# Optimization experiments

Measured on AMD Instinct MI355X. Metric: run time of the kernel, lower is better.

## Reference

```python
import jax, jax.numpy as jnp
import numpy as np

N, E, IN, ED, H, L, OUT = 50000, 600000, 16, 4, 128, 4, 3


def setup_inputs() -> dict:
    key = jax.random.key(0)
    ks = jax.random.split(key, 16)
    s = 0.05  # small init scale for numerical stability
    return {
        "x": jax.random.normal(ks[0], (N, IN), jnp.float32),
        "edge_index": jax.random.randint(ks[1], (2, E), 0, N, jnp.int64 if jax.config.jax_enable_x64 else jnp.int32),
        "edge_attr": jax.random.normal(ks[2], (E, ED), jnp.float32),
        "lin_in_w": jax.random.normal(ks[3], (IN, H), jnp.float32) * s,
        "lin_in_b": jnp.zeros((H,), jnp.float32),
        "msg_w1": jax.random.normal(ks[4], (L, H + ED, H), jnp.float32) * s,
        "msg_b1": jnp.zeros((L, H), jnp.float32),
        "msg_w2": jax.random.normal(ks[5], (L, H, H), jnp.float32) * s,
        "msg_b2": jnp.zeros((L, H), jnp.float32),
        "upd_w1": jax.random.normal(ks[6], (L, 2 * H, H), jnp.float32) * s,
        "upd_b1": jnp.zeros((L, H), jnp.float32),
        "upd_w2": jax.random.normal(ks[7], (L, H, H), jnp.float32) * s,
        "upd_b2": jnp.zeros((L, H), jnp.float32),
        "head_w1": jax.random.normal(ks[8], (H, H), jnp.float32) * s,
        "head_b1": jnp.zeros((H,), jnp.float32),
        "head_w2": jax.random.normal(ks[9], (H, OUT), jnp.float32) * s,
        "head_b2": jnp.zeros((OUT,), jnp.float32),
    }


def reference(x, edge_index, edge_attr, lin_in_w, lin_in_b,
              msg_w1, msg_b1, msg_w2, msg_b2,
              upd_w1, upd_b1, upd_w2, upd_b2,
              head_w1, head_b1, head_w2, head_b2):
    n = x.shape[0]
    src, dst = edge_index[0], edge_index[1]  # PyG: message from src (x_j), aggregate at dst
    h = jax.nn.relu(x @ lin_in_w + lin_in_b)  # [N, H]
    # mean-aggregation denominator (0-degree nodes -> divide by 1, sum is 0 anyway)
    cnt = jax.ops.segment_sum(jnp.ones((src.shape[0],), h.dtype), dst, num_segments=n)
    cnt = jnp.maximum(cnt, 1.0)[:, None]
    for l in range(msg_w1.shape[0]):
        mi = jnp.concatenate([h[src], edge_attr], axis=1)          # [E, H+ED] edge gather
        m = jax.nn.relu(mi @ msg_w1[l] + msg_b1[l])
        m = jax.nn.relu(m @ msg_w2[l] + msg_b2[l])                 # [E, H] per-edge message
        agg = jax.ops.segment_sum(m, dst, num_segments=n) / cnt    # [N, H] scatter-mean
        u = jnp.concatenate([h, agg], axis=1)
        u = jax.nn.relu(u @ upd_w1[l] + upd_b1[l])
        u = u @ upd_w2[l] + upd_b2[l]
        h = jax.nn.relu(u + h)  # residual + relu; dropout is eval-mode identity
    o = jax.nn.relu(h @ head_w1 + head_b1)
    return jax.nn.relu(o @ head_w2 + head_b2)  # [N, OUT]
```

## Files before the change

### kernel.cpp

```cpp
#include <hip/hip_runtime.h>


typedef _Float16 f16x8 __attribute__((ext_vector_type(8)));
typedef _Float16 f16x2 __attribute__((ext_vector_type(2)));
typedef __fp16  fp16x2 __attribute__((ext_vector_type(2)));
typedef float f32x4 __attribute__((ext_vector_type(4)));

__device__ inline uint pk2(float a, float b) {
  fp16x2 h = __builtin_amdgcn_cvt_pkrtz(a, b);
  return __builtin_bit_cast(uint, h);
}
__device__ inline ushort f2h(float f) {
  fp16x2 h = __builtin_amdgcn_cvt_pkrtz(f, 0.f);
  return (ushort)__builtin_bit_cast(uint, h);
}
__device__ inline f16x2 bch(uint u) { return __builtin_bit_cast(f16x2, u); }

template <int NT>
__device__ inline void stage_w(ushort* Ws, const ushort* __restrict__ Wt, int t) {
#pragma unroll
  for (int i = t; i < 2048; i += NT) {
    int r = i >> 4, c = i & 15;
    *(uint4*)&Ws[r * 136 + c * 8] = *(const uint4*)&Wt[r * 128 + c * 8];
  }
}
__device__ inline void mfma_4ks(f32x4* acc, const ushort* A, const ushort* Ws,
                                int wave, int lane) {
  int cl = lane & 15, kq = (lane >> 4) * 8;
  int arow = (wave * 16 + cl) * 136;
#pragma unroll
  for (int ks = 0; ks < 4; ++ks) {
    f16x8 af = *(const f16x8*)&A[arow + ks * 32 + kq];
#pragma unroll
    for (int ct = 0; ct < 8; ++ct) {
      f16x8 bf = *(const f16x8*)&Ws[(ct * 16 + cl) * 136 + ks * 32 + kq];
      acc[ct] = __builtin_amdgcn_mfma_f32_16x16x32_f16(af, bf, acc[ct], 0, 0, 0);
    }
  }
}
__device__ inline void mfma_regA(f32x4* acc, const f16x8* af, const ushort* Ws,
                                 int lane) {
  int cl = lane & 15, kq = (lane >> 4) * 8;
#pragma unroll
  for (int ks = 0; ks < 4; ++ks) {
#pragma unroll
    for (int ct = 0; ct < 8; ++ct) {
      f16x8 bf = *(const f16x8*)&Ws[(ct * 16 + cl) * 136 + ks * 32 + kq];
      acc[ct] = __builtin_amdgcn_mfma_f32_16x16x32_f16(af[ks], bf, acc[ct], 0, 0, 0);
    }
  }
}

__global__ __launch_bounds__(256) void count_int_kernel(const int* __restrict__ dst,
                                                        int* __restrict__ cnti, int E) {
  int e = blockIdx.x * 256 + threadIdx.x;
  if (e < E) atomicAdd(&cnti[dst[e]], 1);
}

__global__ __launch_bounds__(256) void scan_block_sum(const int* __restrict__ cnti,
                                                      int* __restrict__ bsum, int N) {
  int i = blockIdx.x * 256 + threadIdx.x;
  int v = (i < N) ? cnti[i] : 0;
#pragma unroll
  for (int o = 1; o < 64; o <<= 1) v += __shfl_xor(v, o);
  __shared__ int wsum[4];
  if ((threadIdx.x & 63) == 0) wsum[threadIdx.x >> 6] = v;
  __syncthreads();
  if (threadIdx.x == 0) bsum[blockIdx.x] = wsum[0] + wsum[1] + wsum[2] + wsum[3];
}
__global__ __launch_bounds__(256) void scan_partials(int* __restrict__ bsum, int nb) {
  __shared__ int s[256];
  int t = threadIdx.x;
  int v = (t < nb) ? bsum[t] : 0;
  s[t] = v;
  __syncthreads();
  for (int o = 1; o < 256; o <<= 1) {
    int u = (t >= o) ? s[t - o] : 0;
    __syncthreads();
    s[t] += u;
    __syncthreads();
  }
  if (t < nb) bsum[t] = s[t] - v;
}
__global__ __launch_bounds__(256) void scan_final(const int* __restrict__ cnti,
                                                  const int* __restrict__ bsum,
                                                  int* __restrict__ rowptr,
                                                  float* __restrict__ invf, int N) {
  __shared__ int s[256];
  int i = blockIdx.x * 256 + threadIdx.x;
  int t = threadIdx.x;
  int v = (i < N) ? cnti[i] : 0;
  s[t] = v;
  __syncthreads();
  for (int o = 1; o < 256; o <<= 1) {
    int u = (t >= o) ? s[t - o] : 0;
    __syncthreads();
    s[t] += u;
    __syncthreads();
  }
  if (i < N) {
    rowptr[i] = bsum[blockIdx.x] + s[t] - v;
    invf[i] = 1.f / (float)max(v, 1);
  }
}

__global__ __launch_bounds__(256) void scatter_kernel(
    const int* __restrict__ src, const int* __restrict__ dst,
    const float4* __restrict__ ea, const int* __restrict__ rowptr,
    int* __restrict__ tmpc, int* __restrict__ srcs, int* __restrict__ dsts,
    float4* __restrict__ eas, int E) {
  int e = blockIdx.x * 256 + threadIdx.x;
  if (e >= E) return;
  int d = dst[e];
  int r = atomicAdd(&tmpc[d], 1);
  int p = rowptr[d] + r;
  srcs[p] = src[e];
  dsts[p] = d;
  eas[p] = ea[e];
}

struct WPtrs { const float* src[22]; };
__global__ __launch_bounds__(256) void wconv_kernel(WPtrs p, ushort* __restrict__ wtb,
                                                    ushort* __restrict__ wlin) {
  int m = blockIdx.y;
  int idx = blockIdx.x * 256 + threadIdx.x;
  if (m == 21) {
    if (idx >= 4096) return;
    int n = idx >> 5, k = idx & 31;
    wlin[idx] = (k < 16) ? f2h(p.src[21][k * 128 + n]) : (ushort)0;
  } else {
    int n = idx >> 7, k = idx & 127;
    wtb[(size_t)m * 16384 + idx] = f2h(p.src[m][k * 128 + n]);
  }
}

__global__ __launch_bounds__(256) void lin_hw_kernel(
    const float* __restrict__ x, const ushort* __restrict__ wlin,
    const float* __restrict__ lb, const ushort* __restrict__ mw1t,
    const float* __restrict__ mb1, float* __restrict__ h,
    ushort* __restrict__ hwb, int N) {
  __shared__ char smem[69632] __attribute__((aligned(16)));
  ushort* xb  = (ushort*)smem;
  ushort* wsl = (ushort*)(smem + 4096);
  ushort* As1 = (ushort*)(smem + 12288);
  ushort* Ws  = (ushort*)(smem + 34816);
  int t = threadIdx.x, lane = t & 63, wave = t >> 6;
  int m0 = blockIdx.x * 64;
  int cl = lane & 15, kq = (lane >> 4) * 8;

  for (int i = t; i < 2048; i += 256) {
    int row = i >> 5, c = i & 31;
    int m = m0 + row;
    xb[i] = (c < 16 && m < N) ? f2h(x[(size_t)m * 16 + c]) : (ushort)0;
  }
  for (int i = t; i < 4096 / 8; i += 256)
    *(uint4*)&wsl[i * 8] = *(const uint4*)&wlin[i * 8];
  stage_w<256>(Ws, mw1t, t);
  __syncthreads();

  f32x4 acc[8];
#pragma unroll
  for (int i = 0; i < 8; ++i)
#pragma unroll
    for (int j = 0; j < 4; ++j) acc[i][j] = 0.f;
  {
    f16x8 af = *(const f16x8*)&xb[(wave * 16 + cl) * 32 + kq];
#pragma unroll
    for (int ct = 0; ct < 8; ++ct) {
      f16x8 bf = *(const f16x8*)&wsl[(ct * 16 + cl) * 32 + kq];
      acc[ct] = __builtin_amdgcn_mfma_f32_16x16x32_f16(af, bf, acc[ct], 0, 0, 0);
    }
  }
#pragma unroll
  for (int reg = 0; reg < 4; ++reg) {
    int row = wave * 16 + (lane >> 4) * 4 + reg;
    int m = m0 + row;
#pragma unroll
    for (int ct = 0; ct < 8; ++ct) {
      int col = ct * 16 + cl;
      float v = fmaxf(acc[ct][reg] + lb[col], 0.f);
      if (m < N) h[(size_t)m * 128 + col] = v;
      As1[row * 136 + col] = f2h(v);
    }
  }
  __syncthreads();
  f32x4 acc2[8];
#pragma unroll
  for (int i = 0; i < 8; ++i)
#pragma unroll
    for (int j = 0; j < 4; ++j) acc2[i][j] = 0.f;
  mfma_4ks(acc2, As1, Ws, wave, lane);
#pragma unroll
  for (int reg = 0; reg < 4; ++reg) {
    int m = m0 + wave * 16 + (lane >> 4) * 4 + reg;
    if (m >= N) continue;
#pragma unroll
    for (int ct = 0; ct < 8; ++ct) {
      int col = ct * 16 + cl;
      hwb[(size_t)m * 128 + col] = f2h(acc2[ct][reg] + mb1[col]);
    }
  }
}

__global__ __launch_bounds__(256, 4) void edge_kernel_v9(
    const ushort* __restrict__ hw, const float4* __restrict__ eas,
    const int* __restrict__ srcs, const int* __restrict__ dsts,
    const ushort* __restrict__ W2t, const float* __restrict__ Wea,
    const float* __restrict__ b2, float* __restrict__ agg, int E) {
  __shared__ ushort Ws[128 * 136];
  __shared__ uint weaH[64][4];
  __shared__ float b2s[128];
  __shared__ int dss[130];
  int t = threadIdx.x, lane = t & 63, wave = t >> 6;
  int cl = lane & 15, g = lane >> 4;
  int p0 = blockIdx.x * 128;
  int base = wave * 32;

  int e0 = p0 + base + cl, e1 = e0 + 16;
  bool v0 = e0 < E, v1 = e1 < E;
  int s0 = v0 ? srcs[e0] : 0, s1 = v1 ? srcs[e1] : 0;
  float4 ea0 = v0 ? eas[e0] : make_float4(0.f, 0.f, 0.f, 0.f);
  float4 ea1 = v1 ? eas[e1] : make_float4(0.f, 0.f, 0.f, 0.f);
  uint4 hv0[4], hv1[4];
  {
    const ushort* h0 = hw + (size_t)s0 * 128 + g * 8;
    const ushort* h1 = hw + (size_t)s1 * 128 + g * 8;
#pragma unroll
    for (int ks = 0; ks < 4; ++ks) {
      hv0[ks] = v0 ? *(const uint4*)&h0[ks * 32] : make_uint4(0, 0, 0, 0);
      hv1[ks] = v1 ? *(const uint4*)&h1[ks * 32] : make_uint4(0, 0, 0, 0);
    }
  }

  stage_w<256>(Ws, W2t, t);
  if (t < 64) {
    weaH[t][0] = pk2(Wea[2 * t], Wea[2 * t + 1]);
    weaH[t][1] = pk2(Wea[128 + 2 * t], Wea[128 + 2 * t + 1]);
    weaH[t][2] = pk2(Wea[256 + 2 * t], Wea[256 + 2 * t + 1]);
    weaH[t][3] = pk2(Wea[384 + 2 * t], Wea[384 + 2 * t + 1]);
  }
  if (t < 128) {
    b2s[t] = b2[t];
    dss[1 + t] = (p0 + t < E) ? dsts[p0 + t] : -1;
  }
  if (t == 0) dss[0] = (p0 > 0) ? dsts[p0 - 1] : -2;
  if (t == 1) dss[129] = (p0 + 128 < E) ? dsts[p0 + 128] : -3;
  __syncthreads();

  uint e0b[4] = {pk2(ea0.x, ea0.x), pk2(ea0.y, ea0.y), pk2(ea0.z, ea0.z), pk2(ea0.w, ea0.w)};
  uint e1b[4] = {pk2(ea1.x, ea1.x), pk2(ea1.y, ea1.y), pk2(ea1.z, ea1.z), pk2(ea1.w, ea1.w)};

  f16x8 af0[4], af1[4];
  f16x2 z2 = {};
#pragma unroll
  for (int ks = 0; ks < 4; ++ks) {
    union { uint u32[4]; f16x8 v; } o0, o1;
    const uint* q0 = (const uint*)&hv0[ks];
    const uint* q1 = (const uint*)&hv1[ks];
    int k2b = ks * 16 + g * 4;
#pragma unroll
    for (int p = 0; p < 4; ++p) {
      uint4 w4 = *(const uint4*)&weaH[k2b + p][0];
      f16x2 m0h = bch(q0[p]);
      f16x2 m1h = bch(q1[p]);
      m0h += bch(e0b[0]) * bch(w4.x); m1h += bch(e1b[0]) * bch(w4.x);
      m0h += bch(e0b[1]) * bch(w4.y); m1h += bch(e1b[1]) * bch(w4.y);
      m0h += bch(e0b[2]) * bch(w4.z); m1h += bch(e1b[2]) * bch(w4.z);
      m0h += bch(e0b[3]) * bch(w4.w); m1h += bch(e1b[3]) * bch(w4.w);
      o0.u32[p] = __builtin_bit_cast(uint, __builtin_elementwise_max(m0h, z2));
      o1.u32[p] = __builtin_bit_cast(uint, __builtin_elementwise_max(m1h, z2));
    }
    af0[ks] = o0.v; af1[ks] = o1.v;
  }

  f32x4 acc0[8], acc1[8];
#pragma unroll
  for (int i = 0; i < 8; ++i)
#pragma unroll
    for (int j = 0; j < 4; ++j) { acc0[i][j] = 0.f; acc1[i][j] = 0.f; }
#pragma unroll
  for (int ks = 0; ks < 4; ++ks) {
#pragma unroll
    for (int ct = 0; ct < 8; ++ct) {
      f16x8 bf = *(const f16x8*)&Ws[(ct * 16 + cl) * 136 + ks * 32 + g * 8];
      acc0[ct] = __builtin_amdgcn_mfma_f32_16x16x32_f16(af0[ks], bf, acc0[ct], 0, 0, 0);
      acc1[ct] = __builtin_amdgcn_mfma_f32_16x16x32_f16(af1[ks], bf, acc1[ct], 0, 0, 0);
    }
  }

#pragma unroll
  for (int ct = 0; ct < 8; ++ct) {
    float bb = b2s[ct * 16 + cl];
#pragma unroll
    for (int reg = 0; reg < 4; ++reg) {
      acc0[ct][reg] = fmaxf(acc0[ct][reg] + bb, 0.f);
      acc1[ct][reg] = fmaxf(acc1[ct][reg] + bb, 0.f);
    }
  }

  int rloc = lane & 31;
  int dmy = dss[1 + base + rloc];
  int dpv = dss[base + rloc];
  int dafter = dss[1 + base + 32];
  unsigned long long bm = __ballot(dmy != dpv);
  unsigned mask32 = (unsigned)bm | 1u;
  bool firstClosed = ((unsigned)bm & 1u) != 0;
  while (mask32) {
    int rOff = __ffs(mask32) - 1;
    unsigned rest = mask32 & (mask32 - 1);
    int eOff = rest ? (__ffs(rest) - 1) : 32;
    mask32 = rest;
    int d = __shfl(dmy, rOff);
    if (d < 0) continue;
    bool openL = (rOff == 0) && !firstClosed;
    bool openR = (eOff == 32) && (dafter == d);
    float ps[8];
#pragma unroll
    for (int ct = 0; ct < 8; ++ct) ps[ct] = 0.f;
#pragma unroll
    for (int reg = 0; reg < 4; ++reg) {
      int r0w = g * 4 + reg;
      bool in0 = (r0w >= rOff) && (r0w < eOff);
      bool in1 = (r0w + 16 >= rOff) && (r0w + 16 < eOff);
#pragma unroll
      for (int ct = 0; ct < 8; ++ct) {
        if (in0) ps[ct] += acc0[ct][reg];
        if (in1) ps[ct] += acc1[ct][reg];
      }
    }
#pragma unroll
    for (int ct = 0; ct < 8; ++ct) {
      ps[ct] += __shfl_xor(ps[ct], 16);
      ps[ct] += __shfl_xor(ps[ct], 32);
    }
    if (g == 0) {
      float* ag = &agg[(size_t)d * 128 + cl];
      if (openL || openR) {
#pragma unroll
        for (int ct = 0; ct < 8; ++ct) atomicAdd(&ag[ct * 16], ps[ct]);
      } else {
#pragma unroll
        for (int ct = 0; ct < 8; ++ct) ag[ct * 16] = ps[ct];
      }
    }
  }
}

__global__ __launch_bounds__(512, 2) void fused_update(
    const float* __restrict__ h, const float* __restrict__ agg,
    const float* __restrict__ inv, const ushort* __restrict__ Wu1a,
    const ushort* __restrict__ Wu1b, const ushort* __restrict__ Wu2,
    const float* __restrict__ b1, const float* __restrict__ b2,
    const ushort* __restrict__ Wn, const float* __restrict__ bn,
    float* __restrict__ h_out, ushort* __restrict__ hwb,
    const float* __restrict__ hw2, const float* __restrict__ hb2,
    float* __restrict__ out, int N, int is_last) {
  __shared__ char smem[69632] __attribute__((aligned(16)));
  ushort* WsA = (ushort*)smem;
  ushort* WsB = (ushort*)(smem + 34816);
  float* otile = (float*)smem;
  float* w2s   = (float*)(smem + 66560);
  int t = threadIdx.x, lane = t & 63, wave = t >> 6;
  int m0 = blockIdx.x * 128;
  int cl = lane & 15, g = lane >> 4;

  int m2r = m0 + wave * 16 + cl;
  bool mv = m2r < N;
  float sI = mv ? inv[m2r] : 0.f;
  float4 ha[8], ga[8];
  {
    size_t rb = (size_t)(mv ? m2r : 0) * 128 + g * 8;
    const float* hp = h + rb;
    const float* gp = agg + rb;
#pragma unroll
    for (int ks = 0; ks < 4; ++ks) {
      ha[ks * 2 + 0] = *(const float4*)&hp[ks * 32];
      ha[ks * 2 + 1] = *(const float4*)&hp[ks * 32 + 4];
      ga[ks * 2 + 0] = *(const float4*)&gp[ks * 32];
      ga[ks * 2 + 1] = *(const float4*)&gp[ks * 32 + 4];
    }
  }
  stage_w<512>(WsA, Wu1a, t);
  stage_w<512>(WsB, Wu1b, t);
  __syncthreads();

  f16x8 haf[4], af2[4];
#pragma unroll
  for (int ks = 0; ks < 4; ++ks) {
    union { uint u32[4]; f16x8 v; } oh, og;
    const float* fh = (const float*)&ha[ks * 2];
    const float* fg = (const float*)&ga[ks * 2];
#pragma unroll
    for (int j = 0; j < 4; ++j) {
      oh.u32[j] = pk2(fh[j * 2], fh[j * 2 + 1]);
      og.u32[j] = pk2(fg[j * 2] * sI, fg[j * 2 + 1] * sI);
    }
    haf[ks] = oh.v; af2[ks] = og.v;
  }

  f32x4 acc[8];
#pragma unroll
  for (int i = 0; i < 8; ++i)
#pragma unroll
    for (int j = 0; j < 4; ++j) acc[i][j] = 0.f;
  mfma_regA(acc, haf, WsA, lane);
  mfma_regA(acc, af2, WsB, lane);
  __syncthreads();

#pragma unroll
  for (int reg = 0; reg < 4; ++reg) {
    int row = wave * 16 + g * 4 + reg;
#pragma unroll
    for (int ct = 0; ct < 8; ++ct) {
      int col = ct * 16 + cl;
      WsB[row * 136 + col] = f2h(fmaxf(acc[ct][reg] + b1[col], 0.f));
    }
  }
  stage_w<512>(WsA, Wu2, t);
  __syncthreads();

  f32x4 acc2[8];
#pragma unroll
  for (int i = 0; i < 8; ++i)
#pragma unroll
    for (int j = 0; j < 4; ++j) acc2[i][j] = 0.f;
  mfma_4ks(acc2, WsB, WsA, wave, lane);
  __syncthreads();

#pragma unroll
  for (int reg = 0; reg < 4; ++reg) {
    int row = wave * 16 + g * 4 + reg;
    int m = m0 + row;
#pragma unroll
    for (int ct = 0; ct < 8; ++ct) {
      int col = ct * 16 + cl;
      float v = acc2[ct][reg] + b2[col];
      if (m < N) v += h[(size_t)m * 128 + col];
      v = fmaxf(v, 0.f);
      if (!is_last && m < N) h_out[(size_t)m * 128 + col] = v;
      WsB[row * 136 + col] = f2h(v);
    }
  }
  stage_w<512>(WsA, Wn, t);
  __syncthreads();

  f32x4 acc3[8];
#pragma unroll
  for (int i = 0; i < 8; ++i)
#pragma unroll
    for (int j = 0; j < 4; ++j) acc3[i][j] = 0.f;
  mfma_4ks(acc3, WsB, WsA, wave, lane);

  if (!is_last) {
#pragma unroll
    for (int reg = 0; reg < 4; ++reg) {
      int m = m0 + wave * 16 + g * 4 + reg;
      if (m >= N) continue;
#pragma unroll
      for (int ct = 0; ct < 8; ++ct) {
        int col = ct * 16 + cl;
        hwb[(size_t)m * 128 + col] = f2h(acc3[ct][reg] + bn[col]);
      }
    }
  } else {
    __syncthreads();
#pragma unroll
    for (int reg = 0; reg < 4; ++reg) {
      int row = wave * 16 + g * 4 + reg;
#pragma unroll
      for (int ct = 0; ct < 8; ++ct) {
        int col = ct * 16 + cl;
        otile[row * 130 + col] = fmaxf(acc3[ct][reg] + bn[col], 0.f);
      }
    }
    for (int i = t; i < 384; i += 512) w2s[i] = hw2[i];
    __syncthreads();
    if (t < 384) {
      int row = t / 3, c = t % 3;
      int m = m0 + row;
      if (m < N) {
        float s = hb2[c];
#pragma unroll 16
        for (int k = 0; k < 128; ++k) s += otile[row * 130 + k] * w2s[k * 3 + c];
        out[(size_t)m * 3 + c] = fmaxf(s, 0.f);
      }
    }
  }
}

extern "C" void kernel_launch(void* const* d_in, const int* in_sizes, int n_in,
                              void* d_out, int out_size, void* d_ws, size_t ws_size,
                              hipStream_t stream) {
  const float* x       = (const float*)d_in[0];
  const int*   ei      = (const int*)  d_in[1];
  const float* ea      = (const float*)d_in[2];
  const float* lin_w   = (const float*)d_in[3];
  const float* lin_b   = (const float*)d_in[4];
  const float* msg_w1  = (const float*)d_in[5];
  const float* msg_b1  = (const float*)d_in[6];
  const float* msg_w2  = (const float*)d_in[7];
  const float* msg_b2  = (const float*)d_in[8];
  const float* upd_w1  = (const float*)d_in[9];
  const float* upd_b1  = (const float*)d_in[10];
  const float* upd_w2  = (const float*)d_in[11];
  const float* upd_b2  = (const float*)d_in[12];
  const float* head_w1 = (const float*)d_in[13];
  const float* head_b1 = (const float*)d_in[14];
  const float* head_w2 = (const float*)d_in[15];
  const float* head_b2 = (const float*)d_in[16];

  int N = in_sizes[0] / 16;
  int E = in_sizes[1] / 2;
  const int* src = ei;
  const int* dst = ei + E;

  float* ws = (float*)d_ws;
  size_t NH = (size_t)N * 128;
  size_t Nr = ((size_t)N + 4) & ~(size_t)3;
  size_t Er = ((size_t)E + 3) & ~(size_t)3;
  size_t off = 0;
  float*  h    = ws + off; off += NH;
  float*  agg  = ws + off; off += NH;
  float4* eas  = (float4*)(ws + off); off += 4 * Er;
  float*  invf = ws + off; off += Nr;
  ushort* wtb  = (ushort*)(ws + off); off += (size_t)21 * 16384 / 2;
  ushort* wlin = (ushort*)(ws + off); off += 4096 / 2;
  ushort* hwb  = (ushort*)(ws + off); off += NH / 2;
  int*    cnti = (int*)(ws + off); off += Nr;
  int*    tmpc = (int*)(ws + off); off += Nr;
  int*    rowp = (int*)(ws + off); off += Nr;
  int*    srcs = (int*)(ws + off); off += Er;
  int*    dsts = (int*)(ws + off); off += Er;
  int*    bsum = (int*)(ws + off); off += 256;
  float*  out  = (float*)d_out;

  WPtrs wp;
  for (int l = 0; l < 4; ++l) {
    wp.src[l * 5 + 0] = msg_w1 + (size_t)l * 132 * 128;
    wp.src[l * 5 + 1] = msg_w2 + (size_t)l * 128 * 128;
    wp.src[l * 5 + 2] = upd_w1 + (size_t)l * 256 * 128;
    wp.src[l * 5 + 3] = upd_w1 + (size_t)l * 256 * 128 + 128 * 128;
    wp.src[l * 5 + 4] = upd_w2 + (size_t)l * 128 * 128;
  }
  wp.src[20] = head_w1;
  wp.src[21] = lin_w;

  int ngrid = (N + 63) / 64;
  int fgrid = (N + 127) / 128;
  int egrid = (E + 127) / 128;
  int nscan = (N + 255) / 256;

  hipMemsetAsync(cnti, 0, Nr * 4, stream);
  hipMemsetAsync(tmpc, 0, Nr * 4, stream);
  wconv_kernel<<<dim3(64, 22), 256, 0, stream>>>(wp, wtb, wlin);
  count_int_kernel<<<(E + 255) / 256, 256, 0, stream>>>(dst, cnti, E);
  scan_block_sum<<<nscan, 256, 0, stream>>>(cnti, bsum, N);
  scan_partials<<<1, 256, 0, stream>>>(bsum, nscan);
  scan_final<<<nscan, 256, 0, stream>>>(cnti, bsum, rowp, invf, N);
  scatter_kernel<<<(E + 255) / 256, 256, 0, stream>>>(src, dst, (const float4*)ea,
                                                      rowp, tmpc, srcs, dsts, eas, E);
  lin_hw_kernel<<<ngrid, 256, 0, stream>>>(x, wlin, lin_b, wtb, msg_b1, h, hwb, N);

  for (int l = 0; l < 4; ++l) {
    const ushort* mw2t  = wtb + (size_t)(l * 5 + 1) * 16384;
    const ushort* wu1at = wtb + (size_t)(l * 5 + 2) * 16384;
    const ushort* wu1bt = wtb + (size_t)(l * 5 + 3) * 16384;
    const ushort* wu2t  = wtb + (size_t)(l * 5 + 4) * 16384;
    const float*  wea   = msg_w1 + (size_t)l * 132 * 128 + 128 * 128;
    int last = (l == 3);
    const ushort* Wn = last ? (wtb + (size_t)20 * 16384)
                            : (wtb + (size_t)((l + 1) * 5 + 0) * 16384);
    const float* bn = last ? head_b1 : (msg_b1 + (l + 1) * 128);

    hipMemsetAsync(agg, 0, NH * sizeof(float), stream);
    edge_kernel_v9<<<egrid, 256, 0, stream>>>(hwb, eas, srcs, dsts, mw2t, wea,
                                              msg_b2 + l * 128, agg, E);
    fused_update<<<fgrid, 512, 0, stream>>>(h, agg, invf, wu1at, wu1bt, wu2t,
                                            upd_b1 + l * 128, upd_b2 + l * 128,
                                            Wn, bn, h, last ? nullptr : hwb,
                                            head_w2, head_b2, out, N, last);
  }
}
```

Measured before the change: 599.9 us.

## Process two edge tiles per block with prefetched gather for second tile

The edge kernel now handles 256 edges per block in two halves of 128. The second half's source-row gather is issued while the first half is computed, and the first half's MFMA and segment reduction run before the second half is used. This spreads the 128x128 weight staging in LDS over twice as many edges and hides part of the gather latency. The cost is more register pressure under a 4-waves-per-SIMD launch bound, which could cause spills, and half as many blocks, which lowers parallelism.

```diff
diff --git a/kernel.cpp b/kernel.cpp
--- a/kernel.cpp
+++ b/kernel.cpp
@@ -56,7 +56,6 @@
   int e = blockIdx.x * 256 + threadIdx.x;
   if (e < E) atomicAdd(&cnti[dst[e]], 1);
 }
-
 __global__ __launch_bounds__(256) void scan_block_sum(const int* __restrict__ cnti,
                                                       int* __restrict__ bsum, int N) {
   int i = blockIdx.x * 256 + threadIdx.x;
@@ -103,7 +102,6 @@
     invf[i] = 1.f / (float)max(v, 1);
   }
 }
-
 __global__ __launch_bounds__(256) void scatter_kernel(
     const int* __restrict__ src, const int* __restrict__ dst,
     const float4* __restrict__ ea, const int* __restrict__ rowptr,
@@ -202,55 +200,9 @@
   }
 }
 
-__global__ __launch_bounds__(256, 4) void edge_kernel_v9(
-    const ushort* __restrict__ hw, const float4* __restrict__ eas,
-    const int* __restrict__ srcs, const int* __restrict__ dsts,
-    const ushort* __restrict__ W2t, const float* __restrict__ Wea,
-    const float* __restrict__ b2, float* __restrict__ agg, int E) {
-  __shared__ ushort Ws[128 * 136];
-  __shared__ uint weaH[64][4];
-  __shared__ float b2s[128];
-  __shared__ int dss[130];
-  int t = threadIdx.x, lane = t & 63, wave = t >> 6;
-  int cl = lane & 15, g = lane >> 4;
-  int p0 = blockIdx.x * 128;
-  int base = wave * 32;
-
-  int e0 = p0 + base + cl, e1 = e0 + 16;
-  bool v0 = e0 < E, v1 = e1 < E;
-  int s0 = v0 ? srcs[e0] : 0, s1 = v1 ? srcs[e1] : 0;
-  float4 ea0 = v0 ? eas[e0] : make_float4(0.f, 0.f, 0.f, 0.f);
-  float4 ea1 = v1 ? eas[e1] : make_float4(0.f, 0.f, 0.f, 0.f);
-  uint4 hv0[4], hv1[4];
-  {
-    const ushort* h0 = hw + (size_t)s0 * 128 + g * 8;
-    const ushort* h1 = hw + (size_t)s1 * 128 + g * 8;
-#pragma unroll
-    for (int ks = 0; ks < 4; ++ks) {
-      hv0[ks] = v0 ? *(const uint4*)&h0[ks * 32] : make_uint4(0, 0, 0, 0);
-      hv1[ks] = v1 ? *(const uint4*)&h1[ks * 32] : make_uint4(0, 0, 0, 0);
-    }
-  }
-
-  stage_w<256>(Ws, W2t, t);
-  if (t < 64) {
-    weaH[t][0] = pk2(Wea[2 * t], Wea[2 * t + 1]);
-    weaH[t][1] = pk2(Wea[128 + 2 * t], Wea[128 + 2 * t + 1]);
-    weaH[t][2] = pk2(Wea[256 + 2 * t], Wea[256 + 2 * t + 1]);
-    weaH[t][3] = pk2(Wea[384 + 2 * t], Wea[384 + 2 * t + 1]);
-  }
-  if (t < 128) {
-    b2s[t] = b2[t];
-    dss[1 + t] = (p0 + t < E) ? dsts[p0 + t] : -1;
-  }
-  if (t == 0) dss[0] = (p0 > 0) ? dsts[p0 - 1] : -2;
-  if (t == 1) dss[129] = (p0 + 128 < E) ? dsts[p0 + 128] : -3;
-  __syncthreads();
-
-  uint e0b[4] = {pk2(ea0.x, ea0.x), pk2(ea0.y, ea0.y), pk2(ea0.z, ea0.z), pk2(ea0.w, ea0.w)};
-  uint e1b[4] = {pk2(ea1.x, ea1.x), pk2(ea1.y, ea1.y), pk2(ea1.z, ea1.z), pk2(ea1.w, ea1.w)};
-
-  f16x8 af0[4], af1[4];
+__device__ inline void build_m1(f16x8* af0, f16x8* af1, const uint4* hv0,
+                                const uint4* hv1, const uint (*weaH)[4],
+                                const uint* e0b, const uint* e1b, int g) {
   f16x2 z2 = {};
 #pragma unroll
   for (int ks = 0; ks < 4; ++ks) {
@@ -272,8 +224,10 @@
     }
     af0[ks] = o0.v; af1[ks] = o1.v;
   }
-
-  f32x4 acc0[8], acc1[8];
+}
+__device__ inline void mfma_bias(f32x4* acc0, f32x4* acc1, const f16x8* af0,
+                                 const f16x8* af1, const ushort* Ws,
+                                 const float* b2s, int cl, int g) {
 #pragma unroll
   for (int i = 0; i < 8; ++i)
 #pragma unroll
@@ -287,7 +241,6 @@
       acc1[ct] = __builtin_amdgcn_mfma_f32_16x16x32_f16(af1[ks], bf, acc1[ct], 0, 0, 0);
     }
   }
-
 #pragma unroll
   for (int ct = 0; ct < 8; ++ct) {
     float bb = b2s[ct * 16 + cl];
@@ -297,14 +250,13 @@
       acc1[ct][reg] = fmaxf(acc1[ct][reg] + bb, 0.f);
     }
   }
-
-  int rloc = lane & 31;
-  int dmy = dss[1 + base + rloc];
-  int dpv = dss[base + rloc];
-  int dafter = dss[1 + base + 32];
-  unsigned long long bm = __ballot(dmy != dpv);
-  unsigned mask32 = (unsigned)bm | 1u;
-  bool firstClosed = ((unsigned)bm & 1u) != 0;
+}
+__device__ inline void seg_reduce(const f32x4* acc0, const f32x4* acc1,
+                                  int dmy, int dpv, int dafter,
+                                  float* __restrict__ agg, int cl, int g) {
+  unsigned long long bmv = __ballot(dmy != dpv);
+  unsigned mask32 = (unsigned)bmv | 1u;
+  bool firstClosed = ((unsigned)bmv & 1u) != 0;
   while (mask32) {
     int rOff = __ffs(mask32) - 1;
     unsigned rest = mask32 & (mask32 - 1);
@@ -343,6 +295,87 @@
         for (int ct = 0; ct < 8; ++ct) ag[ct * 16] = ps[ct];
       }
     }
+  }
+}
+
+__global__ __launch_bounds__(256, 4) void edge_kernel_v11(
+    const ushort* __restrict__ hw, const float4* __restrict__ eas,
+    const int* __restrict__ srcs, const int* __restrict__ dsts,
+    const ushort* __restrict__ W2t, const float* __restrict__ Wea,
+    const float* __restrict__ b2, float* __restrict__ agg, int E) {
+  __shared__ ushort Ws[128 * 136];
+  __shared__ uint weaH[64][4];
+  __shared__ float b2s[128];
+  __shared__ int dss[258];
+  int t = threadIdx.x, lane = t & 63, wave = t >> 6;
+  int cl = lane & 15, g = lane >> 4;
+  int p0 = blockIdx.x * 256;
+  int base = wave * 32;
+  int rloc = lane & 31;
+
+  int eA0 = p0 + base + cl, eA1 = eA0 + 16;
+  bool vA0 = eA0 < E, vA1 = eA1 < E;
+  int sA0 = vA0 ? srcs[eA0] : 0, sA1 = vA1 ? srcs[eA1] : 0;
+  float4 eaA0 = vA0 ? eas[eA0] : make_float4(0.f, 0.f, 0.f, 0.f);
+  float4 eaA1 = vA1 ? eas[eA1] : make_float4(0.f, 0.f, 0.f, 0.f);
+  uint4 hvA0[4], hvA1[4];
+  {
+    const ushort* h0 = hw + (size_t)sA0 * 128 + g * 8;
+    const ushort* h1 = hw + (size_t)sA1 * 128 + g * 8;
+#pragma unroll
+    for (int ks = 0; ks < 4; ++ks) {
+      hvA0[ks] = vA0 ? *(const uint4*)&h0[ks * 32] : make_uint4(0, 0, 0, 0);
+      hvA1[ks] = vA1 ? *(const uint4*)&h1[ks * 32] : make_uint4(0, 0, 0, 0);
+    }
+  }
+  int eB0 = eA0 + 128, eB1 = eA1 + 128;
+  bool vB0 = eB0 < E, vB1 = eB1 < E;
+  int sB0 = vB0 ? srcs[eB0] : 0, sB1 = vB1 ? srcs[eB1] : 0;
+  float4 eaB0 = vB0 ? eas[eB0] : make_float4(0.f, 0.f, 0.f, 0.f);
+  float4 eaB1 = vB1 ? eas[eB1] : make_float4(0.f, 0.f, 0.f, 0.f);
+
+  stage_w<256>(Ws, W2t, t);
+  if (t < 64) {
+    weaH[t][0] = pk2(Wea[2 * t], Wea[2 * t + 1]);
+    weaH[t][1] = pk2(Wea[128 + 2 * t], Wea[128 + 2 * t + 1]);
+    weaH[t][2] = pk2(Wea[256 + 2 * t], Wea[256 + 2 * t + 1]);
+    weaH[t][3] = pk2(Wea[384 + 2 * t], Wea[384 + 2 * t + 1]);
+  }
+  if (t < 128) b2s[t] = b2[t];
+  dss[1 + t] = (p0 + t < E) ? dsts[p0 + t] : -1;
+  if (t == 0) dss[0] = (p0 > 0) ? dsts[p0 - 1] : -2;
+  if (t == 1) dss[257] = (p0 + 256 < E) ? dsts[p0 + 256] : -3;
+  __syncthreads();
+
+  {
+    uint e0b[4] = {pk2(eaA0.x, eaA0.x), pk2(eaA0.y, eaA0.y), pk2(eaA0.z, eaA0.z), pk2(eaA0.w, eaA0.w)};
+    uint e1b[4] = {pk2(eaA1.x, eaA1.x), pk2(eaA1.y, eaA1.y), pk2(eaA1.z, eaA1.z), pk2(eaA1.w, eaA1.w)};
+    f16x8 af0[4], af1[4];
+    build_m1(af0, af1, hvA0, hvA1, weaH, e0b, e1b, g);
+
+    uint4 hvB0[4], hvB1[4];
+    {
+      const ushort* h0 = hw + (size_t)sB0 * 128 + g * 8;
+      const ushort* h1 = hw + (size_t)sB1 * 128 + g * 8;
+#pragma unroll
+      for (int ks = 0; ks < 4; ++ks) {
+        hvB0[ks] = vB0 ? *(const uint4*)&h0[ks * 32] : make_uint4(0, 0, 0, 0);
+        hvB1[ks] = vB1 ? *(const uint4*)&h1[ks * 32] : make_uint4(0, 0, 0, 0);
+      }
+    }
+
+    f32x4 acc0[8], acc1[8];
+    mfma_bias(acc0, acc1, af0, af1, Ws, b2s, cl, g);
+    seg_reduce(acc0, acc1, dss[1 + base + rloc], dss[base + rloc],
+               dss[1 + base + 32], agg, cl, g);
+
+    uint f0b[4] = {pk2(eaB0.x, eaB0.x), pk2(eaB0.y, eaB0.y), pk2(eaB0.z, eaB0.z), pk2(eaB0.w, eaB0.w)};
+    uint f1b[4] = {pk2(eaB1.x, eaB1.x), pk2(eaB1.y, eaB1.y), pk2(eaB1.z, eaB1.z), pk2(eaB1.w, eaB1.w)};
+    build_m1(af0, af1, hvB0, hvB1, weaH, f0b, f1b, g);
+    mfma_bias(acc0, acc1, af0, af1, Ws, b2s, cl, g);
+    int ob = 128 + base;
+    seg_reduce(acc0, acc1, dss[1 + ob + rloc], dss[ob + rloc],
+               dss[1 + ob + 32], agg, cl, g);
   }
 }
 
@@ -547,7 +580,7 @@
 
   int ngrid = (N + 63) / 64;
   int fgrid = (N + 127) / 128;
-  int egrid = (E + 127) / 128;
+  int egrid = (E + 255) / 256;
   int nscan = (N + 255) / 256;
 
   hipMemsetAsync(cnti, 0, Nr * 4, stream);
@@ -573,8 +606,8 @@
     const float* bn = last ? head_b1 : (msg_b1 + (l + 1) * 128);
 
     hipMemsetAsync(agg, 0, NH * sizeof(float), stream);
-    edge_kernel_v9<<<egrid, 256, 0, stream>>>(hwb, eas, srcs, dsts, mw2t, wea,
-                                              msg_b2 + l * 128, agg, E);
+    edge_kernel_v11<<<egrid, 256, 0, stream>>>(hwb, eas, srcs, dsts, mw2t, wea,
+                                               msg_b2 + l * 128, agg, E);
     fused_update<<<fgrid, 512, 0, stream>>>(h, agg, invf, wu1at, wu1bt, wu2t,
                                             upd_b1 + l * 128, upd_b2 + l * 128,
                                             Wn, bn, h, last ? nullptr : hwb,
```

After: 1.760 ms. 193% more time.
